# Kernel tuning notes

Hardware: AMD Instinct MI355X
Metric: run time of the kernel (lower is better)

## Reference

```python
import jax, jax.numpy as jnp
import numpy as np

WS = 16       # window size
SHIFT = 8     # shift size
HEADS = 16
DIM = 512
HIDDEN = 2048
B, H, W = 8, 64, 64
EPS = 1e-5


def _rel_coords_table(ws):
    h = np.arange(-(ws - 1), ws, dtype=np.float32)
    t = np.stack(np.meshgrid(h, h, indexing='ij'), axis=-1)  # (2ws-1, 2ws-1, 2)
    t = t / (ws - 1) * 8.0
    t = np.sign(t) * np.log2(np.abs(t) + 1.0) / np.log2(8.0)
    return t.reshape(-1, 2)


def _rel_pos_index(ws):
    coords = np.stack(np.meshgrid(np.arange(ws), np.arange(ws), indexing='ij'))
    cf = coords.reshape(2, -1)                      # (2, N)
    rel = (cf[:, :, None] - cf[:, None, :]).transpose(1, 2, 0)  # (N, N, 2)
    rel[..., 0] += ws - 1
    rel[..., 1] += ws - 1
    rel[..., 0] *= 2 * ws - 1
    return rel.sum(-1)                              # (N, N)


def _attn_mask(h, w, ws, shift):
    img = np.zeros((h, w))
    cnt = 0
    for hs in (slice(0, -ws), slice(-ws, -shift), slice(-shift, None)):
        for wsl in (slice(0, -ws), slice(-ws, -shift), slice(-shift, None)):
            img[hs, wsl] = cnt
            cnt += 1
    mw = img.reshape(h // ws, ws, w // ws, ws).transpose(0, 2, 1, 3).reshape(-1, ws * ws)
    am = mw[:, None, :] - mw[:, :, None]            # (nW, N, N)
    return np.where(am != 0, -100.0, 0.0).astype(np.float32)


def _ln(x, g, b):
    m = x.mean(-1, keepdims=True)
    v = ((x - m) ** 2).mean(-1, keepdims=True)
    return (x - m) * jax.lax.rsqrt(v + EPS) * g + b


def setup_inputs() -> dict:
    key = jax.random.key(0)
    ks = jax.random.split(key, 16)
    s = 0.02
    return {
        'x': jax.random.normal(ks[0], (B, H, W, DIM), jnp.float32),
        'qkv_w': jax.random.normal(ks[1], (3 * DIM, DIM), jnp.float32) * s,
        'q_bias': jnp.zeros((DIM,), jnp.float32),
        'v_bias': jnp.zeros((DIM,), jnp.float32),
        'logit_scale': jnp.full((HEADS, 1, 1), np.log(10.0), jnp.float32),
        'cpb_w1': jax.random.normal(ks[2], (512, 2), jnp.float32) * s,
        'cpb_b1': jnp.zeros((512,), jnp.float32),
        'cpb_w2': jax.random.normal(ks[3], (HEADS, 512), jnp.float32) * s,
        'proj_w': jax.random.normal(ks[4], (DIM, DIM), jnp.float32) * s,
        'proj_b': jnp.zeros((DIM,), jnp.float32),
        'norm1_g': jnp.ones((DIM,), jnp.float32),
        'norm1_b': jnp.zeros((DIM,), jnp.float32),
        'norm2_g': jnp.ones((DIM,), jnp.float32),
        'norm2_b': jnp.zeros((DIM,), jnp.float32),
        'fc1_w': jax.random.normal(ks[5], (HIDDEN, DIM), jnp.float32) * s,
        'fc1_b': jnp.zeros((HIDDEN,), jnp.float32),
        'fc2_w': jax.random.normal(ks[6], (DIM, HIDDEN), jnp.float32) * s,
        'fc2_b': jnp.zeros((DIM,), jnp.float32),
    }


def reference(x, qkv_w, q_bias, v_bias, logit_scale, cpb_w1, cpb_b1, cpb_w2,
              proj_w, proj_b, norm1_g, norm1_b, norm2_g, norm2_b,
              fc1_w, fc1_b, fc2_w, fc2_b):
    b, h, w, c = x.shape
    N = WS * WS
    nW = (h // WS) * (w // WS)
    hd = c // HEADS

    # --- shifted window cosine attention ---
    shifted = jnp.roll(x, (-SHIFT, -SHIFT), axis=(1, 2))
    xw = shifted.reshape(b, h // WS, WS, w // WS, WS, c)
    xw = xw.transpose(0, 1, 3, 2, 4, 5).reshape(-1, N, c)  # (b*nW, N, C)

    bias = jnp.concatenate([q_bias, jnp.zeros_like(q_bias), v_bias])
    qkv = (xw @ qkv_w.T + bias).reshape(-1, N, 3, HEADS, hd).transpose(2, 0, 3, 1, 4)
    q, k, v = qkv[0], qkv[1], qkv[2]  # (Bn, heads, N, hd)

    qn = q / jnp.maximum(jnp.linalg.norm(q, axis=-1, keepdims=True), 1e-12)
    kn = k / jnp.maximum(jnp.linalg.norm(k, axis=-1, keepdims=True), 1e-12)
    scale = jnp.exp(jnp.minimum(logit_scale, jnp.log(jnp.float32(100.0))))  # (heads,1,1)
    attn = jnp.einsum('bhnd,bhmd->bhnm', qn, kn) * scale

    # continuous relative position bias (CPB MLP)
    table = jnp.asarray(_rel_coords_table(WS))                    # (M, 2)
    t = jax.nn.relu(table @ cpb_w1.T + cpb_b1) @ cpb_w2.T          # (M, heads)
    idx = _rel_pos_index(WS).reshape(-1)
    rpb = t[idx].reshape(N, N, HEADS).transpose(2, 0, 1)
    rpb = 16.0 * jax.nn.sigmoid(rpb)
    attn = attn + rpb[None]

    mask = jnp.asarray(_attn_mask(h, w, WS, SHIFT))                # (nW, N, N)
    attn = attn.reshape(b, nW, HEADS, N, N) + mask[None, :, None]
    attn = jax.nn.softmax(attn.reshape(-1, HEADS, N, N), axis=-1)

    out = jnp.einsum('bhnm,bhmd->bhnd', attn, v).transpose(0, 2, 1, 3).reshape(-1, N, c)
    out = out @ proj_w.T + proj_b

    out = out.reshape(b, h // WS, w // WS, WS, WS, c)
    out = out.transpose(0, 1, 3, 2, 4, 5).reshape(b, h, w, c)
    out = jnp.roll(out, (SHIFT, SHIFT), axis=(1, 2))

    # post-norm residuals (SwinV2 style)
    x = x + _ln(out, norm1_g, norm1_b)
    hmid = jax.nn.gelu(x @ fc1_w.T + fc1_b, approximate=False)
    mlp_out = hmid @ fc2_w.T + fc2_b
    x = x + _ln(mlp_out, norm2_g, norm2_b)
    return x
```

## Files before the change

### kernel.cpp

```cpp
#include <hip/hip_runtime.h>
#include <math.h>


#define HEADS 16
#define HD 32
#define NTOK 256
#define DIMC 512
#define HIDDEN 2048

typedef __attribute__((ext_vector_type(8))) short bf16x8;
typedef __attribute__((ext_vector_type(4))) float f32x4;
typedef __attribute__((ext_vector_type(8))) unsigned short ushort8;

#define MFMA16(a, b, c) __builtin_amdgcn_mfma_f32_16x16x32_bf16((a), (b), (c), 0, 0, 0)
#define WAIT_VM(N) asm volatile("s_waitcnt vmcnt(" #N ")" ::: "memory")

__device__ __forceinline__ unsigned short f2bf(float f) {
  union { float f; unsigned u; } v; v.f = f;
  unsigned r = v.u + 0x7FFFu + ((v.u >> 16) & 1u);
  return (unsigned short)(r >> 16);
}
__device__ __forceinline__ float bf2f(unsigned short h) {
  union { unsigned u; float f; } v; v.u = ((unsigned)h) << 16; return v.f;
}
__device__ __forceinline__ void gload16(const void* g, void* l) {
  __builtin_amdgcn_global_load_lds(
      (const __attribute__((address_space(1))) unsigned int*)g,
      (__attribute__((address_space(3))) unsigned int*)l, 16, 0, 0);
}
__device__ __forceinline__ int band(int x) { return x < 48 ? 0 : (x < 56 ? 1 : 2); }

__device__ __forceinline__ float gelu_fast(float x) {
  float u2 = x * (1.5957691216f + 0.0713548163f * x * x);
  u2 = fminf(u2, 80.f);
  float e = __expf(u2);
  return x * (e / (e + 1.f));
}

__device__ __forceinline__ void gemm256_main(const unsigned short* Ab, const unsigned short* Bb,
                                             int K, unsigned short* aT, unsigned short* bT,
                                             f32x4 (&acc)[8][4]) {
  const int tid = threadIdx.x;
  const int w = tid >> 6, lane = tid & 63;
  const int cl = lane & 15, g = lane >> 4;
  const int wr = (w >> 2) * 128, wc = (w & 3) * 64;
  const int off0 = (2 * w) * 1024 + lane * 16;
  const int off1 = (2 * w + 1) * 1024 + lane * 16;
  const int r0 = off0 >> 6, c0 = ((off0 >> 4) & 3) ^ ((r0 >> 1) & 3);
  const int r1 = off1 >> 6, c1 = ((off1 >> 4) & 3) ^ ((r1 >> 1) & 3);
  const char* Ac = (const char*)Ab;
  const char* Bc = (const char*)Bb;
  const size_t sA0 = (size_t)r0 * (K * 2) + (size_t)c0 * 16;
  const size_t sA1 = (size_t)r1 * (K * 2) + (size_t)c1 * 16;
  const int T = K >> 5;
#pragma unroll
  for (int p = 0; p < 3; p++) {
    size_t kb = (size_t)p * 64;
    int bo = p * 16384;
    gload16(Ac + sA0 + kb, (char*)aT + bo + off0);
    gload16(Ac + sA1 + kb, (char*)aT + bo + off1);
    gload16(Bc + sA0 + kb, (char*)bT + bo + off0);
    gload16(Bc + sA1 + kb, (char*)bT + bo + off1);
  }
  for (int t = 0; t < T; t++) {
    if (t + 3 <= T) WAIT_VM(8);
    else if (t + 2 == T) WAIT_VM(4);
    else WAIT_VM(0);
    __builtin_amdgcn_s_barrier();
    asm volatile("" ::: "memory");
    if (t + 3 < T) {
      size_t kb = (size_t)(t + 3) * 64;
      int bo = ((t + 3) & 3) * 16384;
      gload16(Ac + sA0 + kb, (char*)aT + bo + off0);
      gload16(Ac + sA1 + kb, (char*)aT + bo + off1);
      gload16(Bc + sA0 + kb, (char*)bT + bo + off0);
      gload16(Bc + sA1 + kb, (char*)bT + bo + off1);
    }
    const int cur = (t & 3) * 8192;
    bf16x8 bfv[4];
#pragma unroll
    for (int ni = 0; ni < 4; ni++) {
      int row = wc + ni * 16 + cl;
      int gs = g ^ ((row >> 1) & 3);
      bfv[ni] = *(const bf16x8*)(bT + cur + row * 32 + gs * 8);
    }
#pragma unroll
    for (int mi = 0; mi < 8; mi++) {
      int row = wr + mi * 16 + cl;
      int gs = g ^ ((row >> 1) & 3);
      bf16x8 af = *(const bf16x8*)(aT + cur + row * 32 + gs * 8);
#pragma unroll
      for (int ni = 0; ni < 4; ni++) acc[mi][ni] = MFMA16(af, bfv[ni], acc[mi][ni]);
    }
  }
}

__device__ __forceinline__ void xcd_swizzle(int& bm, int& bn) {
  int gy = gridDim.y;
  int nwg = gridDim.x * gy;
  int flat = blockIdx.y * gridDim.x + blockIdx.x;
  int cpx = nwg >> 3;
  int swz = (flat & 7) * cpx + (flat >> 3);
  bm = swz / gy;
  bn = swz % gy;
}

__global__ __launch_bounds__(512, 2) void gemm_qkv(const unsigned short* A,
                                                   const unsigned short* Bw, const float* qbias,
                                                   const float* vbias, unsigned short* qo,
                                                   unsigned short* ko, unsigned short* vo) {
  __shared__ unsigned short aT[4 * 8192];
  __shared__ unsigned short bT[4 * 8192];
  int bm, bn;
  xcd_swizzle(bm, bn);
  f32x4 acc[8][4] = {};
  gemm256_main(A + (size_t)bm * 256 * DIMC, Bw + (size_t)bn * 256 * DIMC, DIMC, aT, bT, acc);
  int lane = threadIdx.x & 63, w = threadIdx.x >> 6;
  int wr = (w >> 2) * 128, wc = (w & 3) * 64, g = lane >> 4, cl = lane & 15;
  int which = bn >> 1;
  unsigned short* base = which == 0 ? qo : (which == 1 ? ko : vo);
#pragma unroll
  for (int ni = 0; ni < 4; ni++) {
    int gn = bn * 256 + wc + ni * 16 + cl;
    int wn = gn & 511, head = wn >> 5, hd = wn & 31;
    float bv = (which == 0) ? qbias[wn] : (which == 2 ? vbias[wn] : 0.f);
#pragma unroll
    for (int mi = 0; mi < 8; mi++) {
#pragma unroll
      for (int reg = 0; reg < 4; reg++) {
        int gm = bm * 256 + wr + mi * 16 + 4 * g + reg;
        int win = gm >> 8, tok = gm & 255;
        base[(((size_t)(win * HEADS + head)) * NTOK + tok) * HD + hd] =
            f2bf(acc[mi][ni][reg] + bv);
      }
    }
  }
}

template <int GELU>
__global__ __launch_bounds__(512, 2) void gemm_epi(const unsigned short* A,
                                                   const unsigned short* Bw, const float* bias,
                                                   unsigned short* out, int N, int K) {
  __shared__ unsigned short aT[4 * 8192];
  __shared__ unsigned short bT[4 * 8192];
  int bm, bn;
  xcd_swizzle(bm, bn);
  f32x4 acc[8][4] = {};
  gemm256_main(A + (size_t)bm * 256 * K, Bw + (size_t)bn * 256 * K, K, aT, bT, acc);
  int lane = threadIdx.x & 63, w = threadIdx.x >> 6;
  int wr = (w >> 2) * 128, wc = (w & 3) * 64, g = lane >> 4, cl = lane & 15;
  float bv[4];
#pragma unroll
  for (int ni = 0; ni < 4; ni++) bv[ni] = bias[bn * 256 + wc + ni * 16 + cl];
#pragma unroll
  for (int mi = 0; mi < 8; mi++) {
#pragma unroll
    for (int reg = 0; reg < 4; reg++) {
      int gm = bm * 256 + wr + mi * 16 + 4 * g + reg;
      unsigned short* rowp = out + (size_t)gm * N + bn * 256 + wc + cl;
#pragma unroll
      for (int ni = 0; ni < 4; ni++) {
        float val = acc[mi][ni][reg] + bv[ni];
        if (GELU) val = gelu_fast(val);
        rowp[ni * 16] = f2bf(val);
      }
    }
  }
}

__global__ __launch_bounds__(256) void attn_kernel(const unsigned short* qg,
                                                   const unsigned short* kg,
                                                   const unsigned short* vg, const float* rpbt,
                                                   const float* logit_scale,
                                                   unsigned short* attn_out) {
  __shared__ unsigned short kS[256 * 32];
  __shared__ unsigned short vT[32 * 256];
  __shared__ unsigned short pS[64 * 256];

  int bid = blockIdx.x;
  int qb = bid & 3, h = (bid >> 2) & 15, win = bid >> 6;
  int tid = threadIdx.x, lane = tid & 63, w = tid >> 6;
  int g = lane >> 4, cl = lane & 15;
  const size_t whbase = ((size_t)(win * HEADS + h)) * NTOK * HD;
  const unsigned short* qwin = qg + whbase + (size_t)qb * 64 * HD;
  const unsigned short* kwin = kg + whbase;
  const unsigned short* vwin = vg + whbase;

#pragma unroll
  for (int i = 0; i < 4; i++) {
    int ci = i * 256 + tid, row = ci >> 2, gc = ci & 3;
    uint4 d = *(const uint4*)(kwin + row * 32 + gc * 8);
    *(uint4*)(kS + row * 32 + ((gc ^ ((row >> 1) & 3)) * 8)) = d;
  }
  {
    int tok = tid;
    ushort8 t0 = *(const ushort8*)(vwin + tok * 32);
    ushort8 t1 = *(const ushort8*)(vwin + tok * 32 + 8);
    ushort8 t2 = *(const ushort8*)(vwin + tok * 32 + 16);
    ushort8 t3 = *(const ushort8*)(vwin + tok * 32 + 24);
    int kc = tok >> 3, ki = tok & 7;
#pragma unroll
    for (int j = 0; j < 8; j++) {
      vT[(j)*256 + ((kc ^ (j & 7)) << 3) + ki] = t0[j];
      vT[(8 + j) * 256 + ((kc ^ ((8 + j) & 7)) << 3) + ki] = t1[j];
      vT[(16 + j) * 256 + ((kc ^ ((16 + j) & 7)) << 3) + ki] = t2[j];
      vT[(24 + j) * 256 + ((kc ^ ((24 + j) & 7)) << 3) + ki] = t3[j];
    }
  }
  __syncthreads();

  float scale = __expf(fminf(logit_scale[h], 4.6051702f));

  {
    int row = tid;
    int sw = (row >> 1) & 3;
    ushort8 ch[4];
#pragma unroll
    for (int gc = 0; gc < 4; gc++) ch[gc] = *(const ushort8*)(kS + row * 32 + ((gc ^ sw) * 8));
    float ss = 0.f;
#pragma unroll
    for (int gc = 0; gc < 4; gc++)
#pragma unroll
      for (int j = 0; j < 8; j++) { float f = bf2f(ch[gc][j]); ss += f * f; }
    float rn = rsqrtf(fmaxf(ss, 1e-24f));
#pragma unroll
    for (int gc = 0; gc < 4; gc++) {
      ushort8 o;
#pragma unroll
      for (int j = 0; j < 8; j++) o[j] = f2bf(bf2f(ch[gc][j]) * rn);
      *(ushort8*)(kS + row * 32 + ((gc ^ sw) * 8)) = o;
    }
  }

  bf16x8 qf;
  {
    int qrow = 16 * w + cl;
    ushort8 qraw = *(const ushort8*)(qwin + qrow * 32 + 8 * g);
    float qe[8];
    float ss = 0.f;
#pragma unroll
    for (int j = 0; j < 8; j++) { qe[j] = bf2f(qraw[j]); ss += qe[j] * qe[j]; }
    ss += __shfl_xor(ss, 16, 64);
    ss += __shfl_xor(ss, 32, 64);
    float rn = rsqrtf(fmaxf(ss, 1e-24f)) * scale;
#pragma unroll
    for (int j = 0; j < 8; j++) qf[j] = (short)f2bf(qe[j] * rn);
  }
  __syncthreads();

  f32x4 acc[16];
#pragma unroll
  for (int ct = 0; ct < 16; ct++) {
    int kr = ct * 16 + cl;
    bf16x8 kf = *(const bf16x8*)(kS + kr * 32 + ((g ^ ((kr >> 1) & 3)) * 8));
    f32x4 z = {0.f, 0.f, 0.f, 0.f};
    acc[ct] = MFMA16(qf, kf, z);
  }

  int wh = (win >> 2) & 3, ww = win & 3;
  int bandcc = band(ww * 16 + cl);
  const float* rpbh = rpbt + h * 961;
  float m4[4];
  int baseidx[4], ridq[4];
#pragma unroll
  for (int reg = 0; reg < 4; reg++) {
    int qrow = qb * 64 + 16 * w + 4 * g + reg;
    int ri = qrow >> 4, ci = qrow & 15;
    ridq[reg] = 3 * band(wh * 16 + ri) + band(ww * 16 + ci);
    baseidx[reg] = (ri + 15) * 31 + (ci + 15 - cl);
    m4[reg] = -1e30f;
  }
#pragma unroll
  for (int ct = 0; ct < 16; ct++) {
    int brc = 3 * band(wh * 16 + ct);
#pragma unroll
    for (int reg = 0; reg < 4; reg++) {
      float v = acc[ct][reg] + rpbh[baseidx[reg] - ct * 31] +
                ((ridq[reg] != (brc + bandcc)) ? -100.f : 0.f);
      acc[ct][reg] = v;
      m4[reg] = fmaxf(m4[reg], v);
    }
  }
#pragma unroll
  for (int reg = 0; reg < 4; reg++) {
#pragma unroll
    for (int o = 1; o < 16; o <<= 1) m4[reg] = fmaxf(m4[reg], __shfl_xor(m4[reg], o, 64));
  }

  float s4[4] = {0.f, 0.f, 0.f, 0.f};
#pragma unroll
  for (int ct = 0; ct < 16; ct++) {
#pragma unroll
    for (int reg = 0; reg < 4; reg++) {
      float p = __expf(acc[ct][reg] - m4[reg]);
      s4[reg] += p;
      int row = 16 * w + 4 * g + reg;
      int c = ct * 16 + cl;
      pS[row * 256 + (((c >> 3) ^ (row & 7)) << 3) + (c & 7)] = f2bf(p);
    }
  }
#pragma unroll
  for (int reg = 0; reg < 4; reg++) {
#pragma unroll
    for (int o = 1; o < 16; o <<= 1) s4[reg] += __shfl_xor(s4[reg], o, 64);
  }

  f32x4 o0 = {0.f, 0.f, 0.f, 0.f}, o1 = {0.f, 0.f, 0.f, 0.f};
  int prow = 16 * w + cl;
#pragma unroll
  for (int ks = 0; ks < 8; ks++) {
    bf16x8 pf = *(const bf16x8*)(pS + prow * 256 + ((((ks * 4 + g)) ^ (prow & 7)) << 3));
    int kc = ks * 4 + g;
    bf16x8 vf0 = *(const bf16x8*)(vT + cl * 256 + ((kc ^ (cl & 7)) << 3));
    bf16x8 vf1 = *(const bf16x8*)(vT + (16 + cl) * 256 + ((kc ^ ((16 + cl) & 7)) << 3));
    o0 = MFMA16(pf, vf0, o0);
    o1 = MFMA16(pf, vf1, o1);
  }

#pragma unroll
  for (int reg = 0; reg < 4; reg++) {
    int row = 16 * w + 4 * g + reg;
    float linv = 1.f / s4[reg];
    size_t tokg = (size_t)win * NTOK + qb * 64 + row;
    attn_out[tokg * DIMC + h * 32 + cl] = f2bf(o0[reg] * linv);
    attn_out[tokg * DIMC + h * 32 + 16 + cl] = f2bf(o1[reg] * linv);
  }
}

__global__ __launch_bounds__(256) void cvt_bf16(const float* src, unsigned short* dst, int n8) {
  int i = blockIdx.x * 256 + threadIdx.x;
  if (i >= n8) return;
  const float* s = src + (size_t)i * 8;
  float4 a = *(const float4*)s, b = *(const float4*)(s + 4);
  ushort8 o;
  o[0] = f2bf(a.x); o[1] = f2bf(a.y); o[2] = f2bf(a.z); o[3] = f2bf(a.w);
  o[4] = f2bf(b.x); o[5] = f2bf(b.y); o[6] = f2bf(b.z); o[7] = f2bf(b.w);
  *(ushort8*)(dst + (size_t)i * 8) = o;
}

__device__ __forceinline__ float cpb_coord(int i) {
  float t = (float)(i - 15) * (8.f / 15.f);
  float s = (t > 0.f) ? 1.f : ((t < 0.f) ? -1.f : 0.f);
  return s * log2f(fabsf(t) + 1.f) * (1.f / 3.f);
}

__global__ __launch_bounds__(256) void cpb_kernel(const float* w1, const float* b1, const float* w2,
                                                  float* rpbt) {
  int i = blockIdx.x * 256 + threadIdx.x;
  if (i >= 961 * 16) return;
  int m = i >> 4, h = i & 15;
  int mi = m / 31, mj = m % 31;
  float c0 = cpb_coord(mi), c1 = cpb_coord(mj);
  float acc = 0.f;
  for (int j = 0; j < 512; j++) {
    float hv = fmaxf(w1[2 * j] * c0 + w1[2 * j + 1] * c1 + b1[j], 0.f);
    acc += hv * w2[h * 512 + j];
  }
  rpbt[h * 961 + m] = 16.f / (1.f + __expf(-acc));
}

__global__ __launch_bounds__(256) void xw_gather(const float* x, unsigned short* xw) {
  int idx = blockIdx.x * 256 + threadIdx.x;
  int m = idx >> 6, chunk = idx & 63;
  int win = m >> 8, tok = m & 255;
  int b = win >> 4, wh = (win >> 2) & 3, ww = win & 3;
  int tr = tok >> 4, tc = tok & 15;
  int sr = (wh * 16 + tr + 8) & 63, sc = (ww * 16 + tc + 8) & 63;
  const float* src = x + ((size_t)((b * 64 + sr) * 64 + sc)) * 512 + chunk * 8;
  float4 a = *(const float4*)src, bq = *(const float4*)(src + 4);
  ushort8 o;
  o[0] = f2bf(a.x); o[1] = f2bf(a.y); o[2] = f2bf(a.z); o[3] = f2bf(a.w);
  o[4] = f2bf(bq.x); o[5] = f2bf(bq.y); o[6] = f2bf(bq.z); o[7] = f2bf(bq.w);
  *(ushort8*)(xw + (size_t)m * 512 + chunk * 8) = o;
}

__global__ __launch_bounds__(256) void ln1_kernel(const unsigned short* pr, const float* x,
                                                  const float* gw, const float* bw,
                                                  unsigned short* x1b) {
  int w = threadIdx.x >> 6, lane = threadIdx.x & 63;
  size_t t = (size_t)blockIdx.x * 4 + w;
  int ti = (int)t;
  int b = ti >> 12, rc = ti & 4095, r = rc >> 6, c = rc & 63;
  int sr = (r + 56) & 63, sc = (c + 56) & 63;
  int win = b * 16 + (sr >> 4) * 4 + (sc >> 4);
  int tok = (sr & 15) * 16 + (sc & 15);
  int ch = lane * 8;
  ushort8 pv = *(const ushort8*)(pr + ((size_t)win * 256 + tok) * 512 + ch);
  float pf[8];
  float s = 0.f, s2 = 0.f;
#pragma unroll
  for (int j = 0; j < 8; j++) { pf[j] = bf2f(pv[j]); s += pf[j]; s2 += pf[j] * pf[j]; }
#pragma unroll
  for (int o = 1; o < 64; o <<= 1) { s += __shfl_xor(s, o, 64); s2 += __shfl_xor(s2, o, 64); }
  float mean = s * (1.f / 512.f);
  float rstd = rsqrtf(s2 * (1.f / 512.f) - mean * mean + 1e-5f);
  const float* xrow = x + t * 512 + ch;
  float4 xa = *(const float4*)xrow, xb = *(const float4*)(xrow + 4);
  float xs[8] = {xa.x, xa.y, xa.z, xa.w, xb.x, xb.y, xb.z, xb.w};
  ushort8 o8;
#pragma unroll
  for (int j = 0; j < 8; j++) {
    float y = (pf[j] - mean) * rstd * gw[ch + j] + bw[ch + j];
    o8[j] = f2bf(xs[j] + y);
  }
  *(ushort8*)(x1b + t * 512 + ch) = o8;
}

__global__ __launch_bounds__(256) void ln2_kernel(const unsigned short* mp,
                                                  const unsigned short* x1b, const float* gw,
                                                  const float* bw, float* out) {
  int w = threadIdx.x >> 6, lane = threadIdx.x & 63;
  size_t t = (size_t)blockIdx.x * 4 + w;
  int ch = lane * 8;
  ushort8 mv = *(const ushort8*)(mp + t * 512 + ch);
  float pf[8];
  float s = 0.f, s2 = 0.f;
#pragma unroll
  for (int j = 0; j < 8; j++) { pf[j] = bf2f(mv[j]); s += pf[j]; s2 += pf[j] * pf[j]; }
#pragma unroll
  for (int o = 1; o < 64; o <<= 1) { s += __shfl_xor(s, o, 64); s2 += __shfl_xor(s2, o, 64); }
  float mean = s * (1.f / 512.f);
  float rstd = rsqrtf(s2 * (1.f / 512.f) - mean * mean + 1e-5f);
  ushort8 xv = *(const ushort8*)(x1b + t * 512 + ch);
  float vals[8];
#pragma unroll
  for (int j = 0; j < 8; j++)
    vals[j] = bf2f(xv[j]) + (pf[j] - mean) * rstd * gw[ch + j] + bw[ch + j];
  *(float4*)(out + t * 512 + ch) = make_float4(vals[0], vals[1], vals[2], vals[3]);
  *(float4*)(out + t * 512 + ch + 4) = make_float4(vals[4], vals[5], vals[6], vals[7]);
}

extern "C" void kernel_launch(void* const* d_in, const int* in_sizes, int n_in, void* d_out,
                              int out_size, void* d_ws, size_t ws_size, hipStream_t stream) {
  (void)in_sizes; (void)n_in; (void)out_size; (void)ws_size;
  const float* x = (const float*)d_in[0];
  const float* qkv_w = (const float*)d_in[1];
  const float* q_bias = (const float*)d_in[2];
  const float* v_bias = (const float*)d_in[3];
  const float* logit_sc = (const float*)d_in[4];
  const float* cpb_w1 = (const float*)d_in[5];
  const float* cpb_b1 = (const float*)d_in[6];
  const float* cpb_w2 = (const float*)d_in[7];
  const float* proj_w = (const float*)d_in[8];
  const float* proj_b = (const float*)d_in[9];
  const float* n1g = (const float*)d_in[10];
  const float* n1b = (const float*)d_in[11];
  const float* n2g = (const float*)d_in[12];
  const float* n2b = (const float*)d_in[13];
  const float* fc1_w = (const float*)d_in[14];
  const float* fc1_b = (const float*)d_in[15];
  const float* fc2_w = (const float*)d_in[16];
  const float* fc2_b = (const float*)d_in[17];

  char* ws = (char*)d_ws;
  unsigned short* wq = (unsigned short*)(ws);
  unsigned short* wp = (unsigned short*)(ws + (2ll << 20));
  unsigned short* w1 = (unsigned short*)(ws + (4ll << 20));
  unsigned short* w2 = (unsigned short*)(ws + (8ll << 20));
  float* rpbt = (float*)(ws + (12ll << 20));
  unsigned short* xw = (unsigned short*)(ws + (16ll << 20));
  unsigned short* qbuf = (unsigned short*)(ws + (48ll << 20));
  unsigned short* kbuf = (unsigned short*)(ws + (80ll << 20));
  unsigned short* vbuf = (unsigned short*)(ws + (112ll << 20));
  unsigned short* projout = (unsigned short*)(ws + (144ll << 20));
  unsigned short* x1b = (unsigned short*)(ws + (176ll << 20));
  unsigned short* hmid = (unsigned short*)(ws + (48ll << 20));
  unsigned short* mlpout = xw;
  float* out = (float*)d_out;

  cvt_bf16<<<dim3(384), dim3(256), 0, stream>>>(qkv_w, wq, 1536 * 512 / 8);
  cvt_bf16<<<dim3(128), dim3(256), 0, stream>>>(proj_w, wp, 512 * 512 / 8);
  cvt_bf16<<<dim3(512), dim3(256), 0, stream>>>(fc1_w, w1, 2048 * 512 / 8);
  cvt_bf16<<<dim3(512), dim3(256), 0, stream>>>(fc2_w, w2, 512 * 2048 / 8);
  cpb_kernel<<<dim3(61), dim3(256), 0, stream>>>(cpb_w1, cpb_b1, cpb_w2, rpbt);
  xw_gather<<<dim3(8192), dim3(256), 0, stream>>>(x, xw);

  gemm_qkv<<<dim3(128, 6), dim3(512), 0, stream>>>(xw, wq, q_bias, v_bias, qbuf, kbuf, vbuf);
  attn_kernel<<<dim3(8192), dim3(256), 0, stream>>>(qbuf, kbuf, vbuf, rpbt, logit_sc, xw);
  gemm_epi<0><<<dim3(128, 2), dim3(512), 0, stream>>>(xw, wp, proj_b, projout, 512, 512);
  ln1_kernel<<<dim3(8192), dim3(256), 0, stream>>>(projout, x, n1g, n1b, x1b);

  gemm_epi<1><<<dim3(128, 8), dim3(512), 0, stream>>>(x1b, w1, fc1_b, hmid, 2048, 512);
  gemm_epi<0><<<dim3(128, 2), dim3(512), 0, stream>>>(hmid, w2, fc2_b, mlpout, 512, 2048);
  ln2_kernel<<<dim3(8192), dim3(256), 0, stream>>>(mlpout, x1b, n2g, n2b, out);
}
```

Baseline: 549.8 us.

## Split GEMM main loop into two barrier-separated phases with MFMA priority boosting

The shared GEMM inner loop now runs each k-step as two halves. Each half loads four A fragments (plus all B fragments in the first half), issues half of the next-tile global-to-LDS loads, waits on LDS, and runs a 4x4 MFMA block with raised wave priority, fenced by sched_barriers and extra workgroup barriers. The goal is a ping-pong schedule where memory issue and MFMA bursts alternate across waves, lowering register pressure and improving overlap. The price is two extra s_barriers per iteration and strict ordering that may stall waves.

```diff
diff --git a/kernel.cpp b/kernel.cpp
--- a/kernel.cpp
+++ b/kernel.cpp
@@ -68,30 +68,58 @@
     else WAIT_VM(0);
     __builtin_amdgcn_s_barrier();
     asm volatile("" ::: "memory");
+    const int cur = (t & 3) * 8192;
+    bf16x8 bfv[4], af[4];
+#pragma unroll
+    for (int ni = 0; ni < 4; ni++) {
+      int row = wc + ni * 16 + cl;
+      bfv[ni] = *(const bf16x8*)(bT + cur + row * 32 + ((g ^ ((row >> 1) & 3)) * 8));
+    }
+#pragma unroll
+    for (int mi = 0; mi < 4; mi++) {
+      int row = wr + mi * 16 + cl;
+      af[mi] = *(const bf16x8*)(aT + cur + row * 32 + ((g ^ ((row >> 1) & 3)) * 8));
+    }
     if (t + 3 < T) {
       size_t kb = (size_t)(t + 3) * 64;
       int bo = ((t + 3) & 3) * 16384;
       gload16(Ac + sA0 + kb, (char*)aT + bo + off0);
       gload16(Ac + sA1 + kb, (char*)aT + bo + off1);
+    }
+    asm volatile("s_waitcnt lgkmcnt(0)" ::: "memory");
+    __builtin_amdgcn_sched_barrier(0);
+    __builtin_amdgcn_s_setprio(1);
+#pragma unroll
+    for (int mi = 0; mi < 4; mi++)
+#pragma unroll
+      for (int ni = 0; ni < 4; ni++) acc[mi][ni] = MFMA16(af[mi], bfv[ni], acc[mi][ni]);
+    __builtin_amdgcn_sched_barrier(0);
+    __builtin_amdgcn_s_setprio(0);
+    __builtin_amdgcn_s_barrier();
+    asm volatile("" ::: "memory");
+    bf16x8 af2[4];
+#pragma unroll
+    for (int mi = 0; mi < 4; mi++) {
+      int row = wr + 64 + mi * 16 + cl;
+      af2[mi] = *(const bf16x8*)(aT + cur + row * 32 + ((g ^ ((row >> 1) & 3)) * 8));
+    }
+    if (t + 3 < T) {
+      size_t kb = (size_t)(t + 3) * 64;
+      int bo = ((t + 3) & 3) * 16384;
       gload16(Bc + sA0 + kb, (char*)bT + bo + off0);
       gload16(Bc + sA1 + kb, (char*)bT + bo + off1);
     }
-    const int cur = (t & 3) * 8192;
-    bf16x8 bfv[4];
-#pragma unroll
-    for (int ni = 0; ni < 4; ni++) {
-      int row = wc + ni * 16 + cl;
-      int gs = g ^ ((row >> 1) & 3);
-      bfv[ni] = *(const bf16x8*)(bT + cur + row * 32 + gs * 8);
-    }
-#pragma unroll
-    for (int mi = 0; mi < 8; mi++) {
-      int row = wr + mi * 16 + cl;
-      int gs = g ^ ((row >> 1) & 3);
-      bf16x8 af = *(const bf16x8*)(aT + cur + row * 32 + gs * 8);
-#pragma unroll
-      for (int ni = 0; ni < 4; ni++) acc[mi][ni] = MFMA16(af, bfv[ni], acc[mi][ni]);
-    }
+    asm volatile("s_waitcnt lgkmcnt(0)" ::: "memory");
+    __builtin_amdgcn_sched_barrier(0);
+    __builtin_amdgcn_s_setprio(1);
+#pragma unroll
+    for (int mi = 0; mi < 4; mi++)
+#pragma unroll
+      for (int ni = 0; ni < 4; ni++) acc[4 + mi][ni] = MFMA16(af2[mi], bfv[ni], acc[4 + mi][ni]);
+    __builtin_amdgcn_sched_barrier(0);
+    __builtin_amdgcn_s_setprio(0);
+    __builtin_amdgcn_s_barrier();
+    asm volatile("" ::: "memory");
   }
 }
 
```

Measured after the change: 487.1 us. 1.13x faster.
